# Performance work log

Hardware: AMD Instinct MI355X
Metric: run time of the kernel (lower is better)

## Reference

```python
import jax, jax.numpy as jnp
import numpy as np

B, N, C, H, M, CC = 8, 1024, 1280, 20, 77, 768
FF = 4 * C
AQ_BITS = 8
W_BITS = 8


def fq_sym(x, bits=AQ_BITS):
    # per-tensor symmetric fake quant with straight-through estimator
    qmax = 2.0 ** (bits - 1) - 1.0
    delta = jnp.maximum(jnp.max(jnp.abs(x)), 1e-8) / qmax
    q = jnp.clip(jnp.round(x / delta), -qmax - 1.0, qmax) * delta
    return x + jax.lax.stop_gradient(q - x)


def fq_zero(x, bits=W_BITS):
    # asymmetric, always_zero (zero point = 0): for softmax probs in [0,1]
    levels = 2.0 ** bits - 1.0
    delta = jnp.maximum(jnp.max(x), 1e-8) / levels
    q = jnp.clip(jnp.round(x / delta), 0.0, levels) * delta
    return x + jax.lax.stop_gradient(q - x)


def layer_norm(x, g, b, eps=1e-5):
    mu = jnp.mean(x, axis=-1, keepdims=True)
    var = jnp.var(x, axis=-1, keepdims=True)
    return (x - mu) * jax.lax.rsqrt(var + eps) * g + b


def attention(x, ctx, Wq, Wk, Wv, Wo, bo, heads):
    b, n, c = x.shape
    m = ctx.shape[1]
    dh = c // heads
    q = fq_sym(x @ Wq)
    k = fq_sym(ctx @ Wk)
    v = fq_sym(ctx @ Wv)
    q = q.reshape(b, n, heads, dh).transpose(0, 2, 1, 3)
    k = k.reshape(b, m, heads, dh).transpose(0, 2, 1, 3)
    v = v.reshape(b, m, heads, dh).transpose(0, 2, 1, 3)
    scores = jnp.einsum('bhnd,bhmd->bhnm', q, k) * (dh ** -0.5)
    w = jax.nn.softmax(scores, axis=-1)
    w = fq_zero(w)  # quantized softmax weights (forces explicit prob materialization)
    out = jnp.einsum('bhnm,bhmd->bhnd', w, v)
    out = out.transpose(0, 2, 1, 3).reshape(b, n, c)
    return out @ Wo + bo


def geglu_ff(x, W1, b1, W2, b2):
    h = x @ W1 + b1
    a, g = jnp.split(h, 2, axis=-1)
    return (a * jax.nn.gelu(g)) @ W2 + b2


def setup_inputs() -> dict:
    key = jax.random.key(0)
    ks = jax.random.split(key, 16)
    s = 0.02
    return {
        'x': jax.random.normal(ks[0], (B, N, C), jnp.float32),
        'ctx': jax.random.normal(ks[1], (B, M, CC), jnp.float32),
        'ln1_g': jnp.ones((C,), jnp.float32), 'ln1_b': jnp.zeros((C,), jnp.float32),
        'ln2_g': jnp.ones((C,), jnp.float32), 'ln2_b': jnp.zeros((C,), jnp.float32),
        'ln3_g': jnp.ones((C,), jnp.float32), 'ln3_b': jnp.zeros((C,), jnp.float32),
        'Wq1': jax.random.normal(ks[2], (C, C), jnp.float32) * s,
        'Wk1': jax.random.normal(ks[3], (C, C), jnp.float32) * s,
        'Wv1': jax.random.normal(ks[4], (C, C), jnp.float32) * s,
        'Wo1': jax.random.normal(ks[5], (C, C), jnp.float32) * s,
        'bo1': jnp.zeros((C,), jnp.float32),
        'Wq2': jax.random.normal(ks[6], (C, C), jnp.float32) * s,
        'Wk2': jax.random.normal(ks[7], (CC, C), jnp.float32) * s,
        'Wv2': jax.random.normal(ks[8], (CC, C), jnp.float32) * s,
        'Wo2': jax.random.normal(ks[9], (C, C), jnp.float32) * s,
        'bo2': jnp.zeros((C,), jnp.float32),
        'Wff1': jax.random.normal(ks[10], (C, 2 * FF), jnp.float32) * s,
        'bff1': jnp.zeros((2 * FF,), jnp.float32),
        'Wff2': jax.random.normal(ks[11], (FF, C), jnp.float32) * s,
        'bff2': jnp.zeros((C,), jnp.float32),
        'heads': H,
    }


def reference(x, ctx, ln1_g, ln1_b, ln2_g, ln2_b, ln3_g, ln3_b,
              Wq1, Wk1, Wv1, Wo1, bo1, Wq2, Wk2, Wv2, Wo2, bo2,
              Wff1, bff1, Wff2, bff2, heads):
    h = attention(layer_norm(x, ln1_g, ln1_b), layer_norm(x, ln1_g, ln1_b),
                  Wq1, Wk1, Wv1, Wo1, bo1, heads)
    x = x + h
    h = attention(layer_norm(x, ln2_g, ln2_b), ctx, Wq2, Wk2, Wv2, Wo2, bo2, heads)
    x = x + h
    x = x + geglu_ff(layer_norm(x, ln3_g, ln3_b), Wff1, bff1, Wff2, bff2)
    return x
```

## Files before the change

### kernel.cpp

```cpp
#include <hip/hip_runtime.h>

typedef __attribute__((ext_vector_type(8))) short bf16x8;
typedef __attribute__((ext_vector_type(4))) float f32x4;

#define DEV __device__ __forceinline__
#define MF(A, B, CACC) CACC = __builtin_amdgcn_mfma_f32_16x16x32_bf16(A, B, CACC, 0, 0, 0)

DEV ushort f2b(float f) {
  unsigned u = __float_as_uint(f);
  u += 0x7fffu + ((u >> 16) & 1u);
  return (ushort)(u >> 16);
}
DEV float b2f(ushort u) { return __uint_as_float(((unsigned)u) << 16); }

DEV void gl_lds16(ushort* lds_base, const ushort* gp) {
  __builtin_amdgcn_global_load_lds(
      (__attribute__((address_space(1))) const void*)gp,
      (__attribute__((address_space(3))) void*)lds_base, 16, 0, 0);
}

__global__ void k_zero(unsigned* p, int n) {
  int i = blockIdx.x * blockDim.x + threadIdx.x;
  if (i < n) p[i] = 0u;
}

__global__ __launch_bounds__(256) void k_wt(const float* __restrict__ W,
                                            ushort* __restrict__ WT, int K, int N) {
  __shared__ float T[32][33];
  int k0 = blockIdx.y * 32, n0 = blockIdx.x * 32;
  int tx = threadIdx.x & 31, ty = threadIdx.x >> 5;
  #pragma unroll
  for (int r = ty; r < 32; r += 8) {
    int k = k0 + r, n = n0 + tx;
    T[r][tx] = (k < K && n < N) ? W[(size_t)k * N + n] : 0.f;
  }
  __syncthreads();
  #pragma unroll
  for (int r = ty; r < 32; r += 8) {
    int n = n0 + r, k = k0 + tx;
    if (n < N && k < K) WT[(size_t)n * K + k] = f2b(T[tx][r]);
  }
}

__global__ void k_cvt(const float* __restrict__ in, ushort* __restrict__ out, int n) {
  int i = blockIdx.x * 256 + threadIdx.x;
  if (i < n) out[i] = f2b(in[i]);
}

__global__ __launch_bounds__(256) void k_ln(const float* __restrict__ x,
    const float* __restrict__ g, const float* __restrict__ b,
    ushort* __restrict__ out) {
  const int C = 1280;
  int row = blockIdx.x, tid = threadIdx.x;
  const float* xr = x + (size_t)row * C;
  float v0 = xr[tid], v1 = xr[tid + 256], v2 = xr[tid + 512],
        v3 = xr[tid + 768], v4 = xr[tid + 1024];
  float s = v0 + v1 + v2 + v3 + v4;
  float ss = v0 * v0 + v1 * v1 + v2 * v2 + v3 * v3 + v4 * v4;
  #pragma unroll
  for (int off = 32; off; off >>= 1) {
    s += __shfl_down(s, off);
    ss += __shfl_down(ss, off);
  }
  __shared__ float red[8];
  __shared__ float mu_s, rstd_s;
  int wave = tid >> 6, lane = tid & 63;
  if (lane == 0) { red[wave] = s; red[4 + wave] = ss; }
  __syncthreads();
  if (tid == 0) {
    float S = red[0] + red[1] + red[2] + red[3];
    float SS = red[4] + red[5] + red[6] + red[7];
    float mu = S / C;
    float var = SS / C - mu * mu;
    mu_s = mu;
    rstd_s = rsqrtf(var + 1e-5f);
  }
  __syncthreads();
  float mu = mu_s, rstd = rstd_s;
  size_t o = (size_t)row * C + tid;
  out[o]        = f2b((v0 - mu) * rstd * g[tid]        + b[tid]);
  out[o + 256]  = f2b((v1 - mu) * rstd * g[tid + 256]  + b[tid + 256]);
  out[o + 512]  = f2b((v2 - mu) * rstd * g[tid + 512]  + b[tid + 512]);
  out[o + 768]  = f2b((v3 - mu) * rstd * g[tid + 768]  + b[tid + 768]);
  out[o + 1024] = f2b((v4 - mu) * rstd * g[tid + 1024] + b[tid + 1024]);
}

DEV void st1(float v, int r_, int c_, int ldc, const float* resid,
             float* Cf, ushort* Cb) {
  size_t o = (size_t)r_ * ldc + c_;
  if (resid) v += resid[o];
  if (Cf) Cf[o] = v;
  if (Cb) Cb[o] = f2b(v);
}
DEV float epi4(f32x4 v, int rbase, int c_, int M, int N, int ldc,
               const float* bias, const float* resid, float* Cf, ushort* Cb) {
  float v0 = v.x, v1 = v.y, v2 = v.z, v3 = v.w;
  float am = fmaxf(fmaxf(fabsf(v0), fabsf(v1)), fmaxf(fabsf(v2), fabsf(v3)));
  if (c_ < N) {
    float bb = bias ? bias[c_] : 0.f;
    v0 += bb; v1 += bb; v2 += bb; v3 += bb;
    if (rbase + 0 < M) st1(v0, rbase + 0, c_, ldc, resid, Cf, Cb);
    if (rbase + 1 < M) st1(v1, rbase + 1, c_, ldc, resid, Cf, Cb);
    if (rbase + 2 < M) st1(v2, rbase + 2, c_, ldc, resid, Cf, Cb);
    if (rbase + 3 < M) st1(v3, rbase + 3, c_, ldc, resid, Cf, Cb);
  }
  return am;
}

__global__ __launch_bounds__(256) void k_gemm(
    const ushort* __restrict__ A, int lda,
    const ushort* __restrict__ BT, int ldb,
    float* __restrict__ Cf, ushort* __restrict__ Cb, int ldc,
    const float* __restrict__ bias, const float* __restrict__ resid,
    unsigned* am_slot, int M, int N, int K) {
  __shared__ __align__(16) ushort SAB[8192];
  int tid = threadIdx.x;
  int wave = tid >> 6, lane = tid & 63;
  int q = lane >> 4, mi = lane & 15;
  int wr = (wave >> 1) * 64, wc = (wave & 1) * 64;
  int bm0 = blockIdx.y * 128, bn0 = blockIdx.x * 128;
  f32x4 c00 = {}, c01 = {}, c02 = {}, c03 = {};
  f32x4 c10 = {}, c11 = {}, c12 = {}, c13 = {};
  f32x4 c20 = {}, c21 = {}, c22 = {}, c23 = {};
  f32x4 c30 = {}, c31 = {}, c32 = {}, c33 = {};
  for (int k0 = 0; k0 < K; k0 += 32) {
    __syncthreads();
    #pragma unroll
    for (int t = 0; t < 4; t++) {
      int c = wave * 256 + t * 64 + lane;
      const ushort* gp;
      if (c < 512) {
        int r = c >> 2, kc = (c & 3) << 3;
        int gr = bm0 + r; if (gr >= M) gr = M - 1;
        gp = A + (size_t)gr * lda + k0 + kc;
      } else {
        int c2 = c - 512;
        int r = c2 >> 2, kc = (c2 & 3) << 3;
        int gn = bn0 + r; if (gn >= N) gn = N - 1;
        gp = BT + (size_t)gn * ldb + k0 + kc;
      }
      gl_lds16(&SAB[(wave * 256 + t * 64) * 8], gp);
    }
    __syncthreads();
    const ushort* Ab = &SAB[(wr + mi) * 32 + q * 8];
    const ushort* Bb = &SAB[4096 + (wc + mi) * 32 + q * 8];
    bf16x8 a0 = *(const bf16x8*)(Ab);
    bf16x8 a1 = *(const bf16x8*)(Ab + 512);
    bf16x8 a2 = *(const bf16x8*)(Ab + 1024);
    bf16x8 a3 = *(const bf16x8*)(Ab + 1536);
    bf16x8 b0 = *(const bf16x8*)(Bb);
    bf16x8 b1 = *(const bf16x8*)(Bb + 512);
    bf16x8 b2 = *(const bf16x8*)(Bb + 1024);
    bf16x8 b3 = *(const bf16x8*)(Bb + 1536);
    MF(a0, b0, c00); MF(a0, b1, c01); MF(a0, b2, c02); MF(a0, b3, c03);
    MF(a1, b0, c10); MF(a1, b1, c11); MF(a1, b2, c12); MF(a1, b3, c13);
    MF(a2, b0, c20); MF(a2, b1, c21); MF(a2, b2, c22); MF(a2, b3, c23);
    MF(a3, b0, c30); MF(a3, b1, c31); MF(a3, b2, c32); MF(a3, b3, c33);
  }
  int rb = bm0 + wr + q * 4, cb = bn0 + wc + mi;
  float am = 0.f;
  am = fmaxf(am, epi4(c00, rb +  0, cb +  0, M, N, ldc, bias, resid, Cf, Cb));
  am = fmaxf(am, epi4(c01, rb +  0, cb + 16, M, N, ldc, bias, resid, Cf, Cb));
  am = fmaxf(am, epi4(c02, rb +  0, cb + 32, M, N, ldc, bias, resid, Cf, Cb));
  am = fmaxf(am, epi4(c03, rb +  0, cb + 48, M, N, ldc, bias, resid, Cf, Cb));
  am = fmaxf(am, epi4(c10, rb + 16, cb +  0, M, N, ldc, bias, resid, Cf, Cb));
  am = fmaxf(am, epi4(c11, rb + 16, cb + 16, M, N, ldc, bias, resid, Cf, Cb));
  am = fmaxf(am, epi4(c12, rb + 16, cb + 32, M, N, ldc, bias, resid, Cf, Cb));
  am = fmaxf(am, epi4(c13, rb + 16, cb + 48, M, N, ldc, bias, resid, Cf, Cb));
  am = fmaxf(am, epi4(c20, rb + 32, cb +  0, M, N, ldc, bias, resid, Cf, Cb));
  am = fmaxf(am, epi4(c21, rb + 32, cb + 16, M, N, ldc, bias, resid, Cf, Cb));
  am = fmaxf(am, epi4(c22, rb + 32, cb + 32, M, N, ldc, bias, resid, Cf, Cb));
  am = fmaxf(am, epi4(c23, rb + 32, cb + 48, M, N, ldc, bias, resid, Cf, Cb));
  am = fmaxf(am, epi4(c30, rb + 48, cb +  0, M, N, ldc, bias, resid, Cf, Cb));
  am = fmaxf(am, epi4(c31, rb + 48, cb + 16, M, N, ldc, bias, resid, Cf, Cb));
  am = fmaxf(am, epi4(c32, rb + 48, cb + 32, M, N, ldc, bias, resid, Cf, Cb));
  am = fmaxf(am, epi4(c33, rb + 48, cb + 48, M, N, ldc, bias, resid, Cf, Cb));
  if (am_slot) {
    #pragma unroll
    for (int off = 32; off; off >>= 1) am = fmaxf(am, __shfl_down(am, off));
    if (lane == 0) atomicMax(am_slot, __float_as_uint(am));
  }
}

__global__ void k_quant(const ushort* __restrict__ in, ushort* __restrict__ out,
                        const unsigned* __restrict__ slot, int n) {
  int i = blockIdx.x * 256 + threadIdx.x;
  if (i >= n) return;
  float delta = fmaxf(__uint_as_float(*slot), 1e-8f) * (1.f / 127.f);
  float x = b2f(in[i]);
  float y = fminf(fmaxf(rintf(x / delta), -128.f), 127.f) * delta;
  out[i] = f2b(y);
}

__global__ __launch_bounds__(256) void k_vt(const ushort* __restrict__ vq,
    ushort* __restrict__ vT, int H, int Mr, int Mpad) {
  const int C = 1280;
  __shared__ __align__(16) ushort T[64][72];
  int bh = blockIdx.y, b = bh / H, h = bh % H;
  int m0 = blockIdx.x * 64;
  int tid = threadIdx.x;
  #pragma unroll
  for (int c = tid; c < 512; c += 256) {
    int mm = c >> 3, dc = (c & 7) << 3;
    int m = m0 + mm;
    int4 val = make_int4(0, 0, 0, 0);
    if (m < Mr) val = *(const int4*)(vq + ((size_t)b * Mr + m) * C + h * 64 + dc);
    *(int4*)&T[mm][dc] = val;
  }
  __syncthreads();
  #pragma unroll
  for (int c = tid; c < 512; c += 256) {
    int dd = c >> 3, mc = (c & 7) << 3;
    unsigned w0 = (unsigned)T[mc + 0][dd] | ((unsigned)T[mc + 1][dd] << 16);
    unsigned w1 = (unsigned)T[mc + 2][dd] | ((unsigned)T[mc + 3][dd] << 16);
    unsigned w2 = (unsigned)T[mc + 4][dd] | ((unsigned)T[mc + 5][dd] << 16);
    unsigned w3 = (unsigned)T[mc + 6][dd] | ((unsigned)T[mc + 7][dd] << 16);
    int4 val = make_int4((int)w0, (int)w1, (int)w2, (int)w3);
    *(int4*)(vT + ((size_t)bh * 64 + dd) * Mpad + m0 + mc) = val;
  }
}

__global__ __launch_bounds__(256) void k_attn1(
    const ushort* __restrict__ qq, const ushort* __restrict__ kq,
    float2* __restrict__ rs, unsigned* __restrict__ pmax,
    int H, int N, int Mr, float cs) {
  const int C = 1280;
  __shared__ __align__(16) ushort Qs[64][72];
  __shared__ __align__(16) ushort Ks[64][72];
  int tid = threadIdx.x;
  int wave = tid >> 6, lane = tid & 63;
  int q = lane >> 4, mi = lane & 15;
  int bh = blockIdx.y, b = bh / H, h = bh % H;
  int r0 = blockIdx.x * 64;
  #pragma unroll
  for (int c = tid; c < 512; c += 256) {
    int r = c >> 3, dc = (c & 7) << 3;
    *(int4*)&Qs[r][dc] = *(const int4*)(qq + ((size_t)b * N + r0 + r) * C + h * 64 + dc);
  }
  float m_run = -3.0e38f, z_run = 0.f;
  int nt = (Mr + 63) >> 6;
  for (int mt = 0; mt < nt; mt++) {
    __syncthreads();
    #pragma unroll
    for (int c = tid; c < 512; c += 256) {
      int mm = c >> 3, dc = (c & 7) << 3;
      int m = mt * 64 + mm;
      int4 val = make_int4(0, 0, 0, 0);
      if (m < Mr) val = *(const int4*)(kq + ((size_t)b * Mr + m) * C + h * 64 + dc);
      *(int4*)&Ks[mm][dc] = val;
    }
    __syncthreads();
    f32x4 s0 = {}, s1 = {}, s2 = {}, s3 = {};
    #pragma unroll
    for (int kc = 0; kc < 2; kc++) {
      bf16x8 qv  = *(const bf16x8*)&Qs[wave * 16 + mi][kc * 32 + q * 8];
      bf16x8 k0v = *(const bf16x8*)&Ks[mi][kc * 32 + q * 8];
      bf16x8 k1v = *(const bf16x8*)&Ks[16 + mi][kc * 32 + q * 8];
      bf16x8 k2v = *(const bf16x8*)&Ks[32 + mi][kc * 32 + q * 8];
      bf16x8 k3v = *(const bf16x8*)&Ks[48 + mi][kc * 32 + q * 8];
      MF(k0v, qv, s0); MF(k1v, qv, s1); MF(k2v, qv, s2); MF(k3v, qv, s3);
    }
    int kb = mt * 64 + q * 4;
    float e0  = (kb + 0  < Mr) ? s0.x * cs : -3.0e38f;
    float e1  = (kb + 1  < Mr) ? s0.y * cs : -3.0e38f;
    float e2  = (kb + 2  < Mr) ? s0.z * cs : -3.0e38f;
    float e3  = (kb + 3  < Mr) ? s0.w * cs : -3.0e38f;
    float e4  = (kb + 16 < Mr) ? s1.x * cs : -3.0e38f;
    float e5  = (kb + 17 < Mr) ? s1.y * cs : -3.0e38f;
    float e6  = (kb + 18 < Mr) ? s1.z * cs : -3.0e38f;
    float e7  = (kb + 19 < Mr) ? s1.w * cs : -3.0e38f;
    float e8  = (kb + 32 < Mr) ? s2.x * cs : -3.0e38f;
    float e9  = (kb + 33 < Mr) ? s2.y * cs : -3.0e38f;
    float e10 = (kb + 34 < Mr) ? s2.z * cs : -3.0e38f;
    float e11 = (kb + 35 < Mr) ? s2.w * cs : -3.0e38f;
    float e12 = (kb + 48 < Mr) ? s3.x * cs : -3.0e38f;
    float e13 = (kb + 49 < Mr) ? s3.y * cs : -3.0e38f;
    float e14 = (kb + 50 < Mr) ? s3.z * cs : -3.0e38f;
    float e15 = (kb + 51 < Mr) ? s3.w * cs : -3.0e38f;
    float tm = fmaxf(fmaxf(fmaxf(fmaxf(e0, e1), fmaxf(e2, e3)),
                           fmaxf(fmaxf(e4, e5), fmaxf(e6, e7))),
                     fmaxf(fmaxf(fmaxf(e8, e9), fmaxf(e10, e11)),
                           fmaxf(fmaxf(e12, e13), fmaxf(e14, e15))));
    float mn = fmaxf(m_run, tm);
    float zs = exp2f(e0 - mn)  + exp2f(e1 - mn)  + exp2f(e2 - mn)  + exp2f(e3 - mn)
             + exp2f(e4 - mn)  + exp2f(e5 - mn)  + exp2f(e6 - mn)  + exp2f(e7 - mn)
             + exp2f(e8 - mn)  + exp2f(e9 - mn)  + exp2f(e10 - mn) + exp2f(e11 - mn)
             + exp2f(e12 - mn) + exp2f(e13 - mn) + exp2f(e14 - mn) + exp2f(e15 - mn);
    z_run = z_run * exp2f(m_run - mn) + zs;
    m_run = mn;
  }
  float mo = fmaxf(m_run, __shfl_xor(m_run, 16));
  mo = fmaxf(mo, __shfl_xor(mo, 32));
  float zz = z_run * exp2f(m_run - mo);
  zz += __shfl_xor(zz, 16);
  zz += __shfl_xor(zz, 32);
  if (q == 0) {
    float2 st; st.x = mo; st.y = zz;
    rs[(size_t)bh * N + r0 + wave * 16 + mi] = st;
  }
  float pm = 1.f / zz;
  #pragma unroll
  for (int off = 32; off; off >>= 1) pm = fmaxf(pm, __shfl_down(pm, off));
  if (lane == 0) atomicMax(pmax, __float_as_uint(pm));
}

DEV ushort q8lvl(float s, float cs, float mc) {
  float p = fminf(rintf(exp2f(fmaf(s, cs, -mc))), 255.f);
  return (ushort)(__float_as_uint(p) >> 16);
}

__global__ __launch_bounds__(256) void k_attn2(
    const ushort* __restrict__ qq, const ushort* __restrict__ kq,
    const ushort* __restrict__ vT, const float2* __restrict__ rs,
    const unsigned* __restrict__ pmax, ushort* __restrict__ ao,
    int H, int N, int Mr, int Mpad, float cs) {
  const int C = 1280;
  __shared__ __align__(16) ushort Qs[64][72];
  __shared__ __align__(16) ushort Ks[64][72];
  __shared__ __align__(16) ushort Vs[64][72];
  __shared__ __align__(16) ushort Ps[64][72];
  int tid = threadIdx.x;
  int wave = tid >> 6, lane = tid & 63;
  int q = lane >> 4, mi = lane & 15;
  int bh = blockIdx.y, b = bh / H, h = bh % H;
  int r0 = blockIdx.x * 64;
  #pragma unroll
  for (int c = tid; c < 512; c += 256) {
    int r = c >> 3, dc = (c & 7) << 3;
    *(int4*)&Qs[r][dc] = *(const int4*)(qq + ((size_t)b * N + r0 + r) * C + h * 64 + dc);
  }
  int rbase = wave * 16 + q * 4;
  float delta = fmaxf(__uint_as_float(*pmax), 1e-8f) * (1.f / 255.f);
  float ld = __log2f(delta);
  float2 st0 = rs[(size_t)bh * N + r0 + rbase + 0];
  float2 st1 = rs[(size_t)bh * N + r0 + rbase + 1];
  float2 st2 = rs[(size_t)bh * N + r0 + rbase + 2];
  float2 st3 = rs[(size_t)bh * N + r0 + rbase + 3];
  float mc0 = st0.x + __log2f(st0.y) + ld;
  float mc1 = st1.x + __log2f(st1.y) + ld;
  float mc2 = st2.x + __log2f(st2.y) + ld;
  float mc3 = st3.x + __log2f(st3.y) + ld;
  f32x4 o0 = {}, o1 = {}, o2 = {}, o3 = {};
  int nt = (Mr + 63) >> 6;
  for (int mt = 0; mt < nt; mt++) {
    __syncthreads();
    #pragma unroll
    for (int c = tid; c < 512; c += 256) {
      int mm = c >> 3, dc = (c & 7) << 3;
      int m = mt * 64 + mm;
      int4 val = make_int4(0, 0, 0, 0);
      if (m < Mr) val = *(const int4*)(kq + ((size_t)b * Mr + m) * C + h * 64 + dc);
      *(int4*)&Ks[mm][dc] = val;
      *(int4*)&Vs[mm][dc] = *(const int4*)(vT + ((size_t)bh * 64 + mm) * Mpad + mt * 64 + dc);
    }
    __syncthreads();
    f32x4 s0 = {}, s1 = {}, s2 = {}, s3 = {};
    #pragma unroll
    for (int kc = 0; kc < 2; kc++) {
      bf16x8 aq  = *(const bf16x8*)&Qs[wave * 16 + mi][kc * 32 + q * 8];
      bf16x8 k0v = *(const bf16x8*)&Ks[mi][kc * 32 + q * 8];
      bf16x8 k1v = *(const bf16x8*)&Ks[16 + mi][kc * 32 + q * 8];
      bf16x8 k2v = *(const bf16x8*)&Ks[32 + mi][kc * 32 + q * 8];
      bf16x8 k3v = *(const bf16x8*)&Ks[48 + mi][kc * 32 + q * 8];
      MF(aq, k0v, s0); MF(aq, k1v, s1); MF(aq, k2v, s2); MF(aq, k3v, s3);
    }
    int mlim = Mr - mt * 64;
    bool ok0 = (mi      < mlim);
    bool ok1 = (16 + mi < mlim);
    bool ok2 = (32 + mi < mlim);
    bool ok3 = (48 + mi < mlim);
    Ps[rbase + 0][mi]      = ok0 ? q8lvl(s0.x, cs, mc0) : (ushort)0;
    Ps[rbase + 1][mi]      = ok0 ? q8lvl(s0.y, cs, mc1) : (ushort)0;
    Ps[rbase + 2][mi]      = ok0 ? q8lvl(s0.z, cs, mc2) : (ushort)0;
    Ps[rbase + 3][mi]      = ok0 ? q8lvl(s0.w, cs, mc3) : (ushort)0;
    Ps[rbase + 0][16 + mi] = ok1 ? q8lvl(s1.x, cs, mc0) : (ushort)0;
    Ps[rbase + 1][16 + mi] = ok1 ? q8lvl(s1.y, cs, mc1) : (ushort)0;
    Ps[rbase + 2][16 + mi] = ok1 ? q8lvl(s1.z, cs, mc2) : (ushort)0;
    Ps[rbase + 3][16 + mi] = ok1 ? q8lvl(s1.w, cs, mc3) : (ushort)0;
    Ps[rbase + 0][32 + mi] = ok2 ? q8lvl(s2.x, cs, mc0) : (ushort)0;
    Ps[rbase + 1][32 + mi] = ok2 ? q8lvl(s2.y, cs, mc1) : (ushort)0;
    Ps[rbase + 2][32 + mi] = ok2 ? q8lvl(s2.z, cs, mc2) : (ushort)0;
    Ps[rbase + 3][32 + mi] = ok2 ? q8lvl(s2.w, cs, mc3) : (ushort)0;
    Ps[rbase + 0][48 + mi] = ok3 ? q8lvl(s3.x, cs, mc0) : (ushort)0;
    Ps[rbase + 1][48 + mi] = ok3 ? q8lvl(s3.y, cs, mc1) : (ushort)0;
    Ps[rbase + 2][48 + mi] = ok3 ? q8lvl(s3.z, cs, mc2) : (ushort)0;
    Ps[rbase + 3][48 + mi] = ok3 ? q8lvl(s3.w, cs, mc3) : (ushort)0;
    asm volatile("s_waitcnt lgkmcnt(0)" ::: "memory");
    __builtin_amdgcn_sched_barrier(0);
    #pragma unroll
    for (int kc = 0; kc < 2; kc++) {
      bf16x8 ap = *(const bf16x8*)&Ps[wave * 16 + mi][kc * 32 + q * 8];
      bf16x8 v0 = *(const bf16x8*)&Vs[mi][kc * 32 + q * 8];
      bf16x8 v1 = *(const bf16x8*)&Vs[16 + mi][kc * 32 + q * 8];
      bf16x8 v2 = *(const bf16x8*)&Vs[32 + mi][kc * 32 + q * 8];
      bf16x8 v3 = *(const bf16x8*)&Vs[48 + mi][kc * 32 + q * 8];
      MF(ap, v0, o0); MF(ap, v1, o1); MF(ap, v2, o2); MF(ap, v3, o3);
    }
  }
  int rr = r0 + wave * 16 + q * 4;
  size_t base = ((size_t)b * N + rr) * C + h * 64 + mi;
  ao[base]              = f2b(o0.x * delta); ao[base + C]          = f2b(o0.y * delta);
  ao[base + 2 * C]      = f2b(o0.z * delta); ao[base + 3 * C]      = f2b(o0.w * delta);
  ao[base + 16]         = f2b(o1.x * delta); ao[base + C + 16]     = f2b(o1.y * delta);
  ao[base + 2 * C + 16] = f2b(o1.z * delta); ao[base + 3 * C + 16] = f2b(o1.w * delta);
  ao[base + 32]         = f2b(o2.x * delta); ao[base + C + 32]     = f2b(o2.y * delta);
  ao[base + 2 * C + 32] = f2b(o2.z * delta); ao[base + 3 * C + 32] = f2b(o2.w * delta);
  ao[base + 48]         = f2b(o3.x * delta); ao[base + C + 48]     = f2b(o3.y * delta);
  ao[base + 2 * C + 48] = f2b(o3.z * delta); ao[base + 3 * C + 48] = f2b(o3.w * delta);
}

#define BAR __builtin_amdgcn_s_barrier()
#define LGKM0 do { asm volatile("s_waitcnt lgkmcnt(0)" ::: "memory"); \
                   __builtin_amdgcn_sched_barrier(0); } while (0)
#define VM6 asm volatile("s_waitcnt vmcnt(6)" ::: "memory")
#define VM0 asm volatile("s_waitcnt vmcnt(0)" ::: "memory")
#define PRIO1 __builtin_amdgcn_s_setprio(1)
#define PRIO0 __builtin_amdgcn_s_setprio(0)

#define RDA01(P) do { \
  fa00 = *(const bf16x8*)&(P)[c0];        fa01 = *(const bf16x8*)&(P)[c1]; \
  fa10 = *(const bf16x8*)&(P)[1024 + c0]; fa11 = *(const bf16x8*)&(P)[1024 + c1]; } while (0)
#define RDA23(P) do { \
  fa20 = *(const bf16x8*)&(P)[2048 + c0]; fa21 = *(const bf16x8*)&(P)[2048 + c1]; \
  fa30 = *(const bf16x8*)&(P)[3072 + c0]; fa31 = *(const bf16x8*)&(P)[3072 + c1]; } while (0)
#define RDB(P, H) do { \
  b00 = *(const bf16x8*)&(P)[(H) + c0];        b01 = *(const bf16x8*)&(P)[(H) + c1]; \
  b10 = *(const bf16x8*)&(P)[(H) + 1024 + c0]; b11 = *(const bf16x8*)&(P)[(H) + 1024 + c1]; \
  b20 = *(const bf16x8*)&(P)[(H) + 2048 + c0]; b21 = *(const bf16x8*)&(P)[(H) + 2048 + c1]; \
  b30 = *(const bf16x8*)&(P)[(H) + 3072 + c0]; b31 = *(const bf16x8*)&(P)[(H) + 3072 + c1]; } while (0)
#define RDB8(P) RDB(P, 0)

#define MM8(AX0, AX1, AY0, AY1, C0, C1, C2, C3, D0, D1, D2, D3) \
  MF(AX0, b00, C0); MF(AX1, b01, C0); MF(AX0, b10, C1); MF(AX1, b11, C1); \
  MF(AX0, b20, C2); MF(AX1, b21, C2); MF(AX0, b30, C3); MF(AX1, b31, C3); \
  MF(AY0, b00, D0); MF(AY1, b01, D0); MF(AY0, b10, D1); MF(AY1, b11, D1); \
  MF(AY0, b20, D2); MF(AY1, b21, D2); MF(AY0, b30, D3); MF(AY1, b31, D3)

#define GB8(AP, BP, DB, KT) \
  RDA01(AP); RDB8(BP); \
  stB(DB, KT, 0); stB(DB, KT, 1); stA(DB, KT, 0); \
  BAR; LGKM0; \
  PRIO1; MM8(fa00, fa01, fa10, fa11, c00, c01, c02, c03, c10, c11, c12, c13); PRIO0; \
  BAR; \
  RDA23(AP); \
  stA(DB, KT, 1); stA(DB, KT, 2); stA(DB, KT, 3); \
  BAR; LGKM0; \
  PRIO1; MM8(fa20, fa21, fa30, fa31, c20, c21, c22, c23, c30, c31, c32, c33); PRIO0; \
  VM6; BAR;

#define GT8(AP, BP) \
  RDA01(AP); RDB8(BP); \
  BAR; LGKM0; \
  PRIO1; MM8(fa00, fa01, fa10, fa11, c00, c01, c02, c03, c10, c11, c12, c13); PRIO0; \
  BAR; \
  RDA23(AP); \
  BAR; LGKM0; \
  PRIO1; MM8(fa20, fa21, fa30, fa31, c20, c21, c22, c23, c30, c31, c32, c33); PRIO0;

__global__ __launch_bounds__(512) void k_gemm8(
    const ushort* __restrict__ A, int lda,
    const ushort* __restrict__ BT, int ldb,
    float* __restrict__ Cf, ushort* __restrict__ Cb, int ldc,
    const float* __restrict__ bias, const float* __restrict__ resid,
    unsigned* am_slot, int M, int N, int K) {
  __shared__ __align__(16) ushort SAB[73728];
  int tid = threadIdx.x;
  int wave = tid >> 6, lane = tid & 63;
  int q = lane >> 4, mi = lane & 15;
  int wm = wave >> 1, wn = wave & 1;
  int lr = lane >> 3;
  int lc = ((lane & 7) ^ lr) * 8;

  int NBN = N >> 7;
  int nblk = (M >> 8) * NBN;
  int cpx = nblk >> 3;
  int wg = blockIdx.x;
  int swz = (wg & 7) * cpx + (wg >> 3);
  int bm0 = (swz / NBN) << 8, bn0 = (swz % NBN) << 7;

  const int swzr = (mi & 7) * 8;
  int c0 = (q * 8) ^ swzr, c1 = (32 + q * 8) ^ swzr;
  const ushort* A0p = &SAB[(wm * 64 + mi) * 64];
  const ushort* B0p = &SAB[16384 + (wn * 64 + mi) * 64];
  const ushort* A1p = A0p + 24576; const ushort* B1p = B0p + 24576;
  const ushort* A2p = A0p + 49152; const ushort* B2p = B0p + 49152;

  const ushort* gA = A  + (size_t)(bm0 + wave * 8 + lr) * lda + lc;
  const ushort* gB = BT + (size_t)(bn0 + wave * 8 + lr) * ldb + lc;
  ushort* lA = &SAB[wave * 512];
  ushort* lB = &SAB[16384 + wave * 512];

  auto stA = [&](int bb, int kt, int call) {
    gl_lds16(lA + bb * 24576 + call * 4096,
             gA + (size_t)call * 64 * lda + (size_t)kt * 64);
  };
  auto stB = [&](int bb, int kt, int call) {
    gl_lds16(lB + bb * 24576 + call * 4096,
             gB + (size_t)call * 64 * ldb + (size_t)kt * 64);
  };

  f32x4 c00 = {}, c01 = {}, c02 = {}, c03 = {};
  f32x4 c10 = {}, c11 = {}, c12 = {}, c13 = {};
  f32x4 c20 = {}, c21 = {}, c22 = {}, c23 = {};
  f32x4 c30 = {}, c31 = {}, c32 = {}, c33 = {};
  bf16x8 fa00, fa01, fa10, fa11, fa20, fa21, fa30, fa31;
  bf16x8 b00, b01, b10, b11, b20, b21, b30, b31;

  stB(0, 0, 0); stB(0, 0, 1);
  stA(0, 0, 0); stA(0, 0, 1); stA(0, 0, 2); stA(0, 0, 3);
  stB(1, 1, 0); stB(1, 1, 1);
  stA(1, 1, 0); stA(1, 1, 1); stA(1, 1, 2); stA(1, 1, 3);
  VM6; BAR;

  int NT = K >> 6, NTm = NT - 2;
  for (int t = 0; t < NTm; t += 3) {
    GB8(A0p, B0p, 2, t + 2);
    GB8(A1p, B1p, 0, t + 3);
    GB8(A2p, B2p, 1, t + 4);
  }
  GT8(A0p, B0p);
  VM0; BAR;
  GT8(A1p, B1p);

  int rb = bm0 + wm * 64 + q * 4, cb = bn0 + wn * 64 + mi;
  float am = 0.f;
  am = fmaxf(am, epi4(c00, rb +  0, cb +  0, M, N, ldc, bias, resid, Cf, Cb));
  am = fmaxf(am, epi4(c01, rb +  0, cb + 16, M, N, ldc, bias, resid, Cf, Cb));
  am = fmaxf(am, epi4(c02, rb +  0, cb + 32, M, N, ldc, bias, resid, Cf, Cb));
  am = fmaxf(am, epi4(c03, rb +  0, cb + 48, M, N, ldc, bias, resid, Cf, Cb));
  am = fmaxf(am, epi4(c10, rb + 16, cb +  0, M, N, ldc, bias, resid, Cf, Cb));
  am = fmaxf(am, epi4(c11, rb + 16, cb + 16, M, N, ldc, bias, resid, Cf, Cb));
  am = fmaxf(am, epi4(c12, rb + 16, cb + 32, M, N, ldc, bias, resid, Cf, Cb));
  am = fmaxf(am, epi4(c13, rb + 16, cb + 48, M, N, ldc, bias, resid, Cf, Cb));
  am = fmaxf(am, epi4(c20, rb + 32, cb +  0, M, N, ldc, bias, resid, Cf, Cb));
  am = fmaxf(am, epi4(c21, rb + 32, cb + 16, M, N, ldc, bias, resid, Cf, Cb));
  am = fmaxf(am, epi4(c22, rb + 32, cb + 32, M, N, ldc, bias, resid, Cf, Cb));
  am = fmaxf(am, epi4(c23, rb + 32, cb + 48, M, N, ldc, bias, resid, Cf, Cb));
  am = fmaxf(am, epi4(c30, rb + 48, cb +  0, M, N, ldc, bias, resid, Cf, Cb));
  am = fmaxf(am, epi4(c31, rb + 48, cb + 16, M, N, ldc, bias, resid, Cf, Cb));
  am = fmaxf(am, epi4(c32, rb + 48, cb + 32, M, N, ldc, bias, resid, Cf, Cb));
  am = fmaxf(am, epi4(c33, rb + 48, cb + 48, M, N, ldc, bias, resid, Cf, Cb));
  if (am_slot) {
    #pragma unroll
    for (int off = 32; off; off >>= 1) am = fmaxf(am, __shfl_down(am, off));
    if (lane == 0) atomicMax(am_slot, __float_as_uint(am));
  }
}

DEV ushort ggel(float a, float g) {
  float u = 1.5957691216057308f * g * (1.f + 0.044715f * g * g);
  float s = 1.f / (1.f + __expf(-u));
  return f2b(a * g * s);
}
DEV void epi4g(f32x4 va, f32x4 vg, size_t base, float ba, float bg,
               ushort* __restrict__ GG) {
  GG[base]         = ggel(va.x + ba, vg.x + bg);
  GG[base + 5120]  = ggel(va.y + ba, vg.y + bg);
  GG[base + 10240] = ggel(va.z + ba, vg.z + bg);
  GG[base + 15360] = ggel(va.w + ba, vg.w + bg);
}
#define EPIN(nn, P0, Q0, P1, Q1, P2, Q2, P3, Q3) do { \
  int cg = colBase + nn * 16 + mi; \
  float ba = bias[cg], bg = bias[5120 + cg]; \
  size_t b0_ = (size_t)rowBase * 5120 + cg; \
  epi4g(P0, Q0, b0_,             ba, bg, GG); \
  epi4g(P1, Q1, b0_ + 16 * 5120, ba, bg, GG); \
  epi4g(P2, Q2, b0_ + 32 * 5120, ba, bg, GG); \
  epi4g(P3, Q3, b0_ + 48 * 5120, ba, bg, GG); \
} while (0)

__global__ __launch_bounds__(512) void k_ff1_8p(
    const ushort* __restrict__ A,
    const ushort* __restrict__ BT,
    const float* __restrict__ bias,
    ushort* __restrict__ GG) {
  __shared__ __align__(16) ushort SAB[65536];
  int tid = threadIdx.x;
  int wave = tid >> 6, lane = tid & 63;
  int q = lane >> 4, mi = lane & 15;
  int wm = wave >> 1, wn = wave & 1;
  int lr = lane >> 3;
  int lc = ((lane & 7) ^ lr) * 8;

  int wg = blockIdx.x;
  int swz = (wg & 7) * 160 + (wg >> 3);
  int bm0 = (swz & 31) * 256, bn0 = (swz >> 5) * 128;

  const int swzr = (mi & 7) * 8;
  int c0 = (q * 8) ^ swzr, c1 = (32 + q * 8) ^ swzr;
  const ushort* A0p = &SAB[(wm * 64 + mi) * 64];
  const ushort* B0p = &SAB[16384 + (wn * 64 + mi) * 64];
  const ushort* A1p = A0p + 32768;
  const ushort* B1p = B0p + 32768;

  const ushort* gA  = A  + (size_t)(bm0 + wave * 8 + lr) * 1280 + lc;
  const ushort* gBa = BT + (size_t)(bn0 + wave * 8 + lr) * 1280 + lc;
  const ushort* gBg = BT + (size_t)(5120 + bn0 + wave * 8 + lr) * 1280 + lc;
  ushort* lA = &SAB[wave * 512];
  ushort* lB = &SAB[16384 + wave * 512];

  auto stA = [&](int bb, int kt, int call) {
    gl_lds16(lA + bb * 32768 + call * 4096,
             gA + (size_t)call * 81920 + (size_t)kt * 64);
  };
  auto stBa = [&](int bb, int kt, int call) {
    gl_lds16(lB + bb * 32768 + call * 4096,
             gBa + (size_t)call * 81920 + (size_t)kt * 64);
  };
  auto stBg = [&](int bb, int kt, int call) {
    gl_lds16(lB + bb * 32768 + (call + 2) * 4096,
             gBg + (size_t)call * 81920 + (size_t)kt * 64);
  };

  f32x4 cA00 = {}, cA01 = {}, cA02 = {}, cA03 = {};
  f32x4 cA10 = {}, cA11 = {}, cA12 = {}, cA13 = {};
  f32x4 cA20 = {}, cA21 = {}, cA22 = {}, cA23 = {};
  f32x4 cA30 = {}, cA31 = {}, cA32 = {}, cA33 = {};
  f32x4 cG00 = {}, cG01 = {}, cG02 = {}, cG03 = {};
  f32x4 cG10 = {}, cG11 = {}, cG12 = {}, cG13 = {};
  f32x4 cG20 = {}, cG21 = {}, cG22 = {}, cG23 = {};
  f32x4 cG30 = {}, cG31 = {}, cG32 = {}, cG33 = {};
  bf16x8 fa00, fa01, fa10, fa11, fa20, fa21, fa30, fa31;
  bf16x8 b00, b01, b10, b11, b20, b21, b30, b31;

  stBa(0, 0, 0); stBa(0, 0, 1); stBg(0, 0, 0); stBg(0, 0, 1);
  stA(0, 0, 0); stA(0, 0, 1); stA(0, 0, 2); stA(0, 0, 3);
  stBa(1, 1, 0); stBa(1, 1, 1);
  stA(1, 1, 0); stA(1, 1, 1); stA(1, 1, 2); stA(1, 1, 3);
  VM6; BAR;

  for (int it = 0; it < 10; ++it) {
    int t1 = 2 * it + 1;
    int s0 = t1 + 1; if (s0 > 19) s0 = 19;
    int s1 = t1 + 2; if (s1 > 19) s1 = 19;
    RDA01(A0p); RDB(B0p, 0);
    stBg(1, t1, 0); stBg(1, t1, 1);
    BAR; LGKM0;
    PRIO1; MM8(fa00, fa01, fa10, fa11, cA00, cA01, cA02, cA03,
               cA10, cA11, cA12, cA13); PRIO0;
    BAR;
    RDA23(A0p);
    stBa(0, s0, 0); stBa(0, s0, 1);
    BAR; LGKM0;
    PRIO1; MM8(fa20, fa21, fa30, fa31, cA20, cA21, cA22, cA23,
               cA30, cA31, cA32, cA33); PRIO0;
    BAR;
    RDB(B0p, 8192);
    stA(0, s0, 0); stA(0, s0, 1);
    BAR; LGKM0;
    PRIO1; MM8(fa00, fa01, fa10, fa11, cG00, cG01, cG02, cG03,
               cG10, cG11, cG12, cG13); PRIO0;
    BAR;
    stA(0, s0, 2); stA(0, s0, 3);
    BAR;
    PRIO1; MM8(fa20, fa21, fa30, fa31, cG20, cG21, cG22, cG23,
               cG30, cG31, cG32, cG33); PRIO0;
    VM6; BAR;
    RDA01(A1p); RDB(B1p, 0);
    stBg(0, s0, 0); stBg(0, s0, 1);
    BAR; LGKM0;
    PRIO1; MM8(fa00, fa01, fa10, fa11, cA00, cA01, cA02, cA03,
               cA10, cA11, cA12, cA13); PRIO0;
    BAR;
    RDA23(A1p);
    stBa(1, s1, 0); stBa(1, s1, 1);
    BAR; LGKM0;
    PRIO1; MM8(fa20, fa21, fa30, fa31, cA20, cA21, cA22, cA23,
               cA30, cA31, cA32, cA33); PRIO0;
    BAR;
    RDB(B1p, 8192);
    stA(1, s1, 0); stA(1, s1, 1);
    BAR; LGKM0;
    PRIO1; MM8(fa00, fa01, fa10, fa11, cG00, cG01, cG02, cG03,
               cG10, cG11, cG12, cG13); PRIO0;
    BAR;
    stA(1, s1, 2); stA(1, s1, 3);
    BAR;
    PRIO1; MM8(fa20, fa21, fa30, fa31, cG20, cG21, cG22, cG23,
               cG30, cG31, cG32, cG33); PRIO0;
    VM6; BAR;
  }

  int colBase = bn0 + wn * 64;
  int rowBase = bm0 + wm * 64 + q * 4;
  EPIN(0, cA00, cG00, cA10, cG10, cA20, cG20, cA30, cG30);
  EPIN(1, cA01, cG01, cA11, cG11, cA21, cG21, cA31, cG31);
  EPIN(2, cA02, cG02, cA12, cG12, cA22, cG22, cA32, cG32);
  EPIN(3, cA03, cG03, cA13, cG13, cA23, cG23, cA33, cG33);
}

extern "C" void kernel_launch(void* const* d_in, const int* in_sizes, int n_in,
                              void* d_out, int out_size, void* d_ws, size_t ws_size,
                              hipStream_t stream) {
  const float* x_in = (const float*)d_in[0];
  const float* ctx  = (const float*)d_in[1];
  const float* ln1g = (const float*)d_in[2];
  const float* ln1b = (const float*)d_in[3];
  const float* ln2g = (const float*)d_in[4];
  const float* ln2b = (const float*)d_in[5];
  const float* ln3g = (const float*)d_in[6];
  const float* ln3b = (const float*)d_in[7];
  const float* Wq1  = (const float*)d_in[8];
  const float* Wk1  = (const float*)d_in[9];
  const float* Wv1  = (const float*)d_in[10];
  const float* Wo1  = (const float*)d_in[11];
  const float* bo1  = (const float*)d_in[12];
  const float* Wq2  = (const float*)d_in[13];
  const float* Wk2  = (const float*)d_in[14];
  const float* Wv2  = (const float*)d_in[15];
  const float* Wo2  = (const float*)d_in[16];
  const float* bo2  = (const float*)d_in[17];
  const float* Wff1 = (const float*)d_in[18];
  const float* bff1 = (const float*)d_in[19];
  const float* Wff2 = (const float*)d_in[20];
  const float* bff2 = (const float*)d_in[21];
  float* out = (float*)d_out;

  const int NR = 8192;
  const int C = 1280, H = 20, Nseq = 1024, CC = 768;
  const int MR2 = 616;
  const float CS = 0.18033688011112042f;

  char* ws = (char*)d_ws;
  size_t off = 0;
  auto alloc = [&](size_t bytes) -> void* {
    void* p = ws + off;
    off += (bytes + 255) & ~(size_t)255;
    return p;
  };
  unsigned* scal = (unsigned*)alloc(64);
  ushort* Wq1T  = (ushort*)alloc((size_t)C * C * 2);
  ushort* Wk1T  = (ushort*)alloc((size_t)C * C * 2);
  ushort* Wv1T  = (ushort*)alloc((size_t)C * C * 2);
  ushort* Wo1T  = (ushort*)alloc((size_t)C * C * 2);
  ushort* Wq2T  = (ushort*)alloc((size_t)C * C * 2);
  ushort* Wk2T  = (ushort*)alloc((size_t)C * CC * 2);
  ushort* Wv2T  = (ushort*)alloc((size_t)C * CC * 2);
  ushort* Wo2T  = (ushort*)alloc((size_t)C * C * 2);
  ushort* WF1T  = (ushort*)alloc((size_t)10240 * C * 2);
  ushort* WF2T  = (ushort*)alloc((size_t)C * 5120 * 2);
  ushort* LN    = (ushort*)alloc((size_t)NR * C * 2);
  size_t regionR = off;
  ushort* QQ    = (ushort*)alloc((size_t)NR * C * 2);
  ushort* KQ    = (ushort*)alloc((size_t)NR * C * 2);
  ushort* VQ    = (ushort*)alloc((size_t)NR * C * 2);
  ushort* VT    = (ushort*)alloc((size_t)160 * 64 * 1024 * 2);
  float2* RS    = (float2*)alloc((size_t)160 * 1024 * 8);
  ushort* CTXB  = (ushort*)alloc((size_t)MR2 * CC * 2);
  size_t need = off;
  ushort* AO = VQ;
  ushort* GG = (ushort*)(ws + regionR);
  if (ws_size < need) return;

  k_zero<<<1, 64, 0, stream>>>(scal, 8);
  k_wt<<<dim3(40, 40), 256, 0, stream>>>(Wq1, Wq1T, C, C);
  k_wt<<<dim3(40, 40), 256, 0, stream>>>(Wk1, Wk1T, C, C);
  k_wt<<<dim3(40, 40), 256, 0, stream>>>(Wv1, Wv1T, C, C);
  k_wt<<<dim3(40, 40), 256, 0, stream>>>(Wo1, Wo1T, C, C);
  k_wt<<<dim3(40, 40), 256, 0, stream>>>(Wq2, Wq2T, C, C);
  k_wt<<<dim3(40, 24), 256, 0, stream>>>(Wk2, Wk2T, CC, C);
  k_wt<<<dim3(40, 24), 256, 0, stream>>>(Wv2, Wv2T, CC, C);
  k_wt<<<dim3(40, 40), 256, 0, stream>>>(Wo2, Wo2T, C, C);
  k_wt<<<dim3(320, 40), 256, 0, stream>>>(Wff1, WF1T, C, 10240);
  k_wt<<<dim3(40, 160), 256, 0, stream>>>(Wff2, WF2T, 5120, C);

  k_ln<<<NR, 256, 0, stream>>>(x_in, ln1g, ln1b, LN);
  k_gemm8<<<dim3(320), 512, 0, stream>>>(LN, C, Wq1T, C, nullptr, QQ, C,
                                         nullptr, nullptr, scal + 0, NR, C, C);
  k_quant<<<(NR * C + 255) / 256, 256, 0, stream>>>(QQ, QQ, scal + 0, NR * C);
  k_gemm8<<<dim3(320), 512, 0, stream>>>(LN, C, Wk1T, C, nullptr, KQ, C,
                                         nullptr, nullptr, scal + 1, NR, C, C);
  k_quant<<<(NR * C + 255) / 256, 256, 0, stream>>>(KQ, KQ, scal + 1, NR * C);
  k_gemm8<<<dim3(320), 512, 0, stream>>>(LN, C, Wv1T, C, nullptr, VQ, C,
                                         nullptr, nullptr, scal + 2, NR, C, C);
  k_quant<<<(NR * C + 255) / 256, 256, 0, stream>>>(VQ, VQ, scal + 2, NR * C);
  k_vt<<<dim3(16, 160), 256, 0, stream>>>(VQ, VT, H, 1024, 1024);
  k_attn1<<<dim3(16, 160), 256, 0, stream>>>(QQ, KQ, RS, scal + 3, H, Nseq, 1024, CS);
  k_attn2<<<dim3(16, 160), 256, 0, stream>>>(QQ, KQ, VT, RS, scal + 3, AO,
                                             H, Nseq, 1024, 1024, CS);
  k_gemm8<<<dim3(320), 512, 0, stream>>>(AO, C, Wo1T, C, out, nullptr, C,
                                         bo1, x_in, nullptr, NR, C, C);

  k_ln<<<NR, 256, 0, stream>>>(out, ln2g, ln2b, LN);
  k_gemm8<<<dim3(320), 512, 0, stream>>>(LN, C, Wq2T, C, nullptr, QQ, C,
                                         nullptr, nullptr, scal + 4, NR, C, C);
  k_quant<<<(NR * C + 255) / 256, 256, 0, stream>>>(QQ, QQ, scal + 4, NR * C);
  k_cvt<<<(MR2 * CC + 255) / 256, 256, 0, stream>>>(ctx, CTXB, MR2 * CC);
  k_gemm<<<dim3(10, 5), 256, 0, stream>>>(CTXB, CC, Wk2T, CC, nullptr, KQ, C,
                                          nullptr, nullptr, scal + 5, MR2, C, CC);
  k_quant<<<(MR2 * C + 255) / 256, 256, 0, stream>>>(KQ, KQ, scal + 5, MR2 * C);
  k_gemm<<<dim3(10, 5), 256, 0, stream>>>(CTXB, CC, Wv2T, CC, nullptr, VQ, C,
                                          nullptr, nullptr, scal + 6, MR2, C, CC);
  k_quant<<<(MR2 * C + 255) / 256, 256, 0, stream>>>(VQ, VQ, scal + 6, MR2 * C);
  k_vt<<<dim3(2, 160), 256, 0, stream>>>(VQ, VT, H, 77, 128);
  k_attn1<<<dim3(16, 160), 256, 0, stream>>>(QQ, KQ, RS, scal + 7, H, Nseq, 77, CS);
  k_attn2<<<dim3(16, 160), 256, 0, stream>>>(QQ, KQ, VT, RS, scal + 7, AO,
                                             H, Nseq, 77, 128, CS);
  k_gemm8<<<dim3(320), 512, 0, stream>>>(AO, C, Wo2T, C, out, nullptr, C,
                                         bo2, out, nullptr, NR, C, C);

  k_ln<<<NR, 256, 0, stream>>>(out, ln3g, ln3b, LN);
  k_ff1_8p<<<dim3(1280), 512, 0, stream>>>(LN, WF1T, bff1, GG);
  k_gemm8<<<dim3(320), 512, 0, stream>>>(GG, 5120, WF2T, 5120, out, nullptr, C,
                                         bff2, out, nullptr, NR, C, 5120);
}
```

Baseline: 1.742 ms.

## Fuse Q/K/V projections into one wide GEMM with per-slice absmax scales

```diff
diff --git a/kernel.cpp b/kernel.cpp
--- a/kernel.cpp
+++ b/kernel.cpp
@@ -112,7 +112,7 @@
     const ushort* __restrict__ BT, int ldb,
     float* __restrict__ Cf, ushort* __restrict__ Cb, int ldc,
     const float* __restrict__ bias, const float* __restrict__ resid,
-    unsigned* am_slot, int M, int N, int K) {
+    unsigned* am_slot, int M, int N, int K, int slcN) {
   __shared__ __align__(16) ushort SAB[8192];
   int tid = threadIdx.x;
   int wave = tid >> 6, lane = tid & 63;
@@ -178,23 +178,25 @@
   if (am_slot) {
     #pragma unroll
     for (int off = 32; off; off >>= 1) am = fmaxf(am, __shfl_down(am, off));
-    if (lane == 0) atomicMax(am_slot, __float_as_uint(am));
-  }
-}
-
-__global__ void k_quant(const ushort* __restrict__ in, ushort* __restrict__ out,
-                        const unsigned* __restrict__ slot, int n) {
+    if (lane == 0) atomicMax(am_slot + bn0 / slcN, __float_as_uint(am));
+  }
+}
+
+__global__ void k_quant3(const ushort* __restrict__ in, ushort* __restrict__ out,
+                         const unsigned* __restrict__ slotb, int n,
+                         int colw, int ld, int slcw) {
   int i = blockIdx.x * 256 + threadIdx.x;
   if (i >= n) return;
-  float delta = fmaxf(__uint_as_float(*slot), 1e-8f) * (1.f / 127.f);
-  float x = b2f(in[i]);
+  int row = i / colw, col = i - row * colw;
+  size_t a = (size_t)row * ld + col;
+  float delta = fmaxf(__uint_as_float(slotb[col / slcw]), 1e-8f) * (1.f / 127.f);
+  float x = b2f(in[a]);
   float y = fminf(fmaxf(rintf(x / delta), -128.f), 127.f) * delta;
-  out[i] = f2b(y);
+  out[a] = f2b(y);
 }
 
 __global__ __launch_bounds__(256) void k_vt(const ushort* __restrict__ vq,
-    ushort* __restrict__ vT, int H, int Mr, int Mpad) {
-  const int C = 1280;
+    ushort* __restrict__ vT, int H, int Mr, int Mpad, int ldv) {
   __shared__ __align__(16) ushort T[64][72];
   int bh = blockIdx.y, b = bh / H, h = bh % H;
   int m0 = blockIdx.x * 64;
@@ -204,7 +206,7 @@
     int mm = c >> 3, dc = (c & 7) << 3;
     int m = m0 + mm;
     int4 val = make_int4(0, 0, 0, 0);
-    if (m < Mr) val = *(const int4*)(vq + ((size_t)b * Mr + m) * C + h * 64 + dc);
+    if (m < Mr) val = *(const int4*)(vq + ((size_t)b * Mr + m) * ldv + h * 64 + dc);
     *(int4*)&T[mm][dc] = val;
   }
   __syncthreads();
@@ -223,8 +225,7 @@
 __global__ __launch_bounds__(256) void k_attn1(
     const ushort* __restrict__ qq, const ushort* __restrict__ kq,
     float2* __restrict__ rs, unsigned* __restrict__ pmax,
-    int H, int N, int Mr, float cs) {
-  const int C = 1280;
+    int H, int N, int Mr, int ldq, int ldk, float cs) {
   __shared__ __align__(16) ushort Qs[64][72];
   __shared__ __align__(16) ushort Ks[64][72];
   int tid = threadIdx.x;
@@ -235,7 +236,7 @@
   #pragma unroll
   for (int c = tid; c < 512; c += 256) {
     int r = c >> 3, dc = (c & 7) << 3;
-    *(int4*)&Qs[r][dc] = *(const int4*)(qq + ((size_t)b * N + r0 + r) * C + h * 64 + dc);
+    *(int4*)&Qs[r][dc] = *(const int4*)(qq + ((size_t)b * N + r0 + r) * ldq + h * 64 + dc);
   }
   float m_run = -3.0e38f, z_run = 0.f;
   int nt = (Mr + 63) >> 6;
@@ -246,7 +247,7 @@
       int mm = c >> 3, dc = (c & 7) << 3;
       int m = mt * 64 + mm;
       int4 val = make_int4(0, 0, 0, 0);
-      if (m < Mr) val = *(const int4*)(kq + ((size_t)b * Mr + m) * C + h * 64 + dc);
+      if (m < Mr) val = *(const int4*)(kq + ((size_t)b * Mr + m) * ldk + h * 64 + dc);
       *(int4*)&Ks[mm][dc] = val;
     }
     __syncthreads();
@@ -313,7 +314,7 @@
     const ushort* __restrict__ qq, const ushort* __restrict__ kq,
     const ushort* __restrict__ vT, const float2* __restrict__ rs,
     const unsigned* __restrict__ pmax, ushort* __restrict__ ao,
-    int H, int N, int Mr, int Mpad, float cs) {
+    int H, int N, int Mr, int Mpad, int ldq, int ldk, float cs) {
   const int C = 1280;
   __shared__ __align__(16) ushort Qs[64][72];
   __shared__ __align__(16) ushort Ks[64][72];
@@ -327,7 +328,7 @@
   #pragma unroll
   for (int c = tid; c < 512; c += 256) {
     int r = c >> 3, dc = (c & 7) << 3;
-    *(int4*)&Qs[r][dc] = *(const int4*)(qq + ((size_t)b * N + r0 + r) * C + h * 64 + dc);
+    *(int4*)&Qs[r][dc] = *(const int4*)(qq + ((size_t)b * N + r0 + r) * ldq + h * 64 + dc);
   }
   int rbase = wave * 16 + q * 4;
   float delta = fmaxf(__uint_as_float(*pmax), 1e-8f) * (1.f / 255.f);
@@ -349,7 +350,7 @@
       int mm = c >> 3, dc = (c & 7) << 3;
       int m = mt * 64 + mm;
       int4 val = make_int4(0, 0, 0, 0);
-      if (m < Mr) val = *(const int4*)(kq + ((size_t)b * Mr + m) * C + h * 64 + dc);
+      if (m < Mr) val = *(const int4*)(kq + ((size_t)b * Mr + m) * ldk + h * 64 + dc);
       *(int4*)&Ks[mm][dc] = val;
       *(int4*)&Vs[mm][dc] = *(const int4*)(vT + ((size_t)bh * 64 + mm) * Mpad + mt * 64 + dc);
     }
@@ -462,7 +463,7 @@
     const ushort* __restrict__ BT, int ldb,
     float* __restrict__ Cf, ushort* __restrict__ Cb, int ldc,
     const float* __restrict__ bias, const float* __restrict__ resid,
-    unsigned* am_slot, int M, int N, int K) {
+    unsigned* am_slot, int M, int N, int K, int slcN) {
   __shared__ __align__(16) ushort SAB[73728];
   int tid = threadIdx.x;
   int wave = tid >> 6, lane = tid & 63;
@@ -543,7 +544,7 @@
   if (am_slot) {
     #pragma unroll
     for (int off = 32; off; off >>= 1) am = fmaxf(am, __shfl_down(am, off));
-    if (lane == 0) atomicMax(am_slot, __float_as_uint(am));
+    if (lane == 0) atomicMax(am_slot + bn0 / slcN, __float_as_uint(am));
   }
 }
 
@@ -741,14 +742,13 @@
   ushort* WF2T  = (ushort*)alloc((size_t)C * 5120 * 2);
   ushort* LN    = (ushort*)alloc((size_t)NR * C * 2);
   size_t regionR = off;
-  ushort* QQ    = (ushort*)alloc((size_t)NR * C * 2);
-  ushort* KQ    = (ushort*)alloc((size_t)NR * C * 2);
-  ushort* VQ    = (ushort*)alloc((size_t)NR * C * 2);
+  ushort* QKV   = (ushort*)alloc((size_t)NR * 3840 * 2);
   ushort* VT    = (ushort*)alloc((size_t)160 * 64 * 1024 * 2);
   float2* RS    = (float2*)alloc((size_t)160 * 1024 * 8);
   ushort* CTXB  = (ushort*)alloc((size_t)MR2 * CC * 2);
+  ushort* KV2   = (ushort*)alloc((size_t)MR2 * 2560 * 2);
   size_t need = off;
-  ushort* AO = VQ;
+  ushort* AO = LN;
   ushort* GG = (ushort*)(ws + regionR);
   if (ws_size < need) return;
 
@@ -765,42 +765,38 @@
   k_wt<<<dim3(40, 160), 256, 0, stream>>>(Wff2, WF2T, 5120, C);
 
   k_ln<<<NR, 256, 0, stream>>>(x_in, ln1g, ln1b, LN);
-  k_gemm8<<<dim3(320), 512, 0, stream>>>(LN, C, Wq1T, C, nullptr, QQ, C,
-                                         nullptr, nullptr, scal + 0, NR, C, C);
-  k_quant<<<(NR * C + 255) / 256, 256, 0, stream>>>(QQ, QQ, scal + 0, NR * C);
-  k_gemm8<<<dim3(320), 512, 0, stream>>>(LN, C, Wk1T, C, nullptr, KQ, C,
-                                         nullptr, nullptr, scal + 1, NR, C, C);
-  k_quant<<<(NR * C + 255) / 256, 256, 0, stream>>>(KQ, KQ, scal + 1, NR * C);
-  k_gemm8<<<dim3(320), 512, 0, stream>>>(LN, C, Wv1T, C, nullptr, VQ, C,
-                                         nullptr, nullptr, scal + 2, NR, C, C);
-  k_quant<<<(NR * C + 255) / 256, 256, 0, stream>>>(VQ, VQ, scal + 2, NR * C);
-  k_vt<<<dim3(16, 160), 256, 0, stream>>>(VQ, VT, H, 1024, 1024);
-  k_attn1<<<dim3(16, 160), 256, 0, stream>>>(QQ, KQ, RS, scal + 3, H, Nseq, 1024, CS);
-  k_attn2<<<dim3(16, 160), 256, 0, stream>>>(QQ, KQ, VT, RS, scal + 3, AO,
-                                             H, Nseq, 1024, 1024, CS);
+  k_gemm8<<<dim3(960), 512, 0, stream>>>(LN, C, Wq1T, C, nullptr, QKV, 3840,
+                                         nullptr, nullptr, scal + 0, NR, 3840, C, 1280);
+  k_quant3<<<(NR * 3840 + 255) / 256, 256, 0, stream>>>(QKV, QKV, scal + 0,
+                                                        NR * 3840, 3840, 3840, 1280);
+  k_vt<<<dim3(16, 160), 256, 0, stream>>>(QKV + 2560, VT, H, 1024, 1024, 3840);
+  k_attn1<<<dim3(16, 160), 256, 0, stream>>>(QKV, QKV + 1280, RS, scal + 3,
+                                             H, Nseq, 1024, 3840, 3840, CS);
+  k_attn2<<<dim3(16, 160), 256, 0, stream>>>(QKV, QKV + 1280, VT, RS, scal + 3, AO,
+                                             H, Nseq, 1024, 1024, 3840, 3840, CS);
   k_gemm8<<<dim3(320), 512, 0, stream>>>(AO, C, Wo1T, C, out, nullptr, C,
-                                         bo1, x_in, nullptr, NR, C, C);
+                                         bo1, x_in, nullptr, NR, C, C, C);
 
   k_ln<<<NR, 256, 0, stream>>>(out, ln2g, ln2b, LN);
-  k_gemm8<<<dim3(320), 512, 0, stream>>>(LN, C, Wq2T, C, nullptr, QQ, C,
-                                         nullptr, nullptr, scal + 4, NR, C, C);
-  k_quant<<<(NR * C + 255) / 256, 256, 0, stream>>>(QQ, QQ, scal + 4, NR * C);
+  k_gemm8<<<dim3(320), 512, 0, stream>>>(LN, C, Wq2T, C, nullptr, QKV, 3840,
+                                         nullptr, nullptr, scal + 4, NR, C, C, C);
+  k_quant3<<<(NR * C + 255) / 256, 256, 0, stream>>>(QKV, QKV, scal + 4,
+                                                     NR * C, 1280, 3840, 1280);
   k_cvt<<<(MR2 * CC + 255) / 256, 256, 0, stream>>>(ctx, CTXB, MR2 * CC);
-  k_gemm<<<dim3(10, 5), 256, 0, stream>>>(CTXB, CC, Wk2T, CC, nullptr, KQ, C,
-                                          nullptr, nullptr, scal + 5, MR2, C, CC);
-  k_quant<<<(MR2 * C + 255) / 256, 256, 0, stream>>>(KQ, KQ, scal + 5, MR2 * C);
-  k_gemm<<<dim3(10, 5), 256, 0, stream>>>(CTXB, CC, Wv2T, CC, nullptr, VQ, C,
-                                          nullptr, nullptr, scal + 6, MR2, C, CC);
-  k_quant<<<(MR2 * C + 255) / 256, 256, 0, stream>>>(VQ, VQ, scal + 6, MR2 * C);
-  k_vt<<<dim3(2, 160), 256, 0, stream>>>(VQ, VT, H, 77, 128);
-  k_attn1<<<dim3(16, 160), 256, 0, stream>>>(QQ, KQ, RS, scal + 7, H, Nseq, 77, CS);
-  k_attn2<<<dim3(16, 160), 256, 0, stream>>>(QQ, KQ, VT, RS, scal + 7, AO,
-                                             H, Nseq, 77, 128, CS);
+  k_gemm<<<dim3(20, 5), 256, 0, stream>>>(CTXB, CC, Wk2T, CC, nullptr, KV2, 2560,
+                                          nullptr, nullptr, scal + 5, MR2, 2560, CC, 1280);
+  k_quant3<<<(MR2 * 2560 + 255) / 256, 256, 0, stream>>>(KV2, KV2, scal + 5,
+                                                         MR2 * 2560, 2560, 2560, 1280);
+  k_vt<<<dim3(2, 160), 256, 0, stream>>>(KV2 + 1280, VT, H, 77, 128, 2560);
+  k_attn1<<<dim3(16, 160), 256, 0, stream>>>(QKV, KV2, RS, scal + 7,
+                                             H, Nseq, 77, 3840, 2560, CS);
+  k_attn2<<<dim3(16, 160), 256, 0, stream>>>(QKV, KV2, VT, RS, scal + 7, AO,
+                                             H, Nseq, 77, 128, 3840, 2560, CS);
   k_gemm8<<<dim3(320), 512, 0, stream>>>(AO, C, Wo2T, C, out, nullptr, C,
-                                         bo2, out, nullptr, NR, C, C);
+                                         bo2, out, nullptr, NR, C, C, C);
 
   k_ln<<<NR, 256, 0, stream>>>(out, ln3g, ln3b, LN);
   k_ff1_8p<<<dim3(1280), 512, 0, stream>>>(LN, WF1T, bff1, GG);
   k_gemm8<<<dim3(320), 512, 0, stream>>>(GG, 5120, WF2T, 5120, out, nullptr, C,
-                                         bff2, out, nullptr, NR, C, 5120);
-}
+                                         bff2, out, nullptr, NR, C, 5120, C);
+}
```

Result: faster. 1.686 ms (-3.2%).
